# Performance work log

Hardware: AMD Instinct MI355X
Metric: run time of the kernel (lower is better)

The kernel has to match this reference:

```python
import jax, jax.numpy as jnp
import numpy as np

N = 50000
TOPK = 32
IN_C = 128
OUT_C = 64
NEG_SLOPE = 0.2
BN_EPS = 1e-5


def setup_inputs() -> dict:
    key = jax.random.key(0)
    ks = jax.random.split(key, 8)
    x = jax.random.normal(ks[0], (N, IN_C), dtype=jnp.float32)
    embedding = jax.random.normal(ks[1], (N, OUT_C), dtype=jnp.float32)
    # edges: each node has TOPK incoming edges, no self loops
    tgt = jnp.repeat(jnp.arange(N, dtype=jnp.int64), TOPK)
    off = jax.random.randint(ks[2], (N * TOPK,), 1, N, dtype=jnp.int64)
    src = (tgt + off) % N
    edge_index = jnp.stack([src, tgt], axis=0)
    lin_w = jax.random.normal(ks[3], (OUT_C, IN_C), dtype=jnp.float32) * (1.0 / np.sqrt(IN_C))
    att_i = jax.random.normal(ks[4], (1, 1, OUT_C), dtype=jnp.float32) * 0.1
    att_j = jax.random.normal(ks[5], (1, 1, OUT_C), dtype=jnp.float32) * 0.1
    att_em_i = jax.random.normal(ks[6], (1, 1, OUT_C), dtype=jnp.float32) * 0.1
    att_em_j = jax.random.normal(ks[7], (1, 1, OUT_C), dtype=jnp.float32) * 0.1
    bias = jnp.zeros((OUT_C,), dtype=jnp.float32)
    bn_gamma = jnp.ones((OUT_C,), dtype=jnp.float32)
    bn_beta = jnp.zeros((OUT_C,), dtype=jnp.float32)
    return {"x": x, "embedding": embedding, "edge_index": edge_index,
            "lin_w": lin_w, "att_i": att_i, "att_j": att_j,
            "att_em_i": att_em_i, "att_em_j": att_em_j, "bias": bias,
            "bn_gamma": bn_gamma, "bn_beta": bn_beta}


def _gnn_forward(x, embedding, lin_w, att_i, att_j, att_em_i, att_em_j,
                 bias, bn_gamma, bn_beta, src, tgt):
    n = x.shape[0]
    # linear transform: [N, heads=1, OUT_C]
    x_lin = (x @ lin_w.T).reshape(n, 1, OUT_C)
    # gather per edge (self loops already appended to src/tgt)
    x_i = x_lin[tgt]                      # [Etot, 1, C]
    x_j = x_lin[src]                      # [Etot, 1, C]
    emb_i = embedding[tgt][:, None, :]    # [Etot, 1, C]
    emb_j = embedding[src][:, None, :]
    # attention logits, eq (6)-(8)
    alpha = ((x_i * att_i).sum(-1) + (emb_i * att_em_i).sum(-1)
             + (x_j * att_j).sum(-1) + (emb_j * att_em_j).sum(-1))  # [Etot, 1]
    alpha = jnp.where(alpha >= 0, alpha, NEG_SLOPE * alpha)
    # segment softmax over incoming edges of each target node
    m = jax.ops.segment_max(alpha, tgt, num_segments=n)
    m = jnp.where(jnp.isfinite(m), m, 0.0)
    e = jnp.exp(alpha - m[tgt])
    denom = jax.ops.segment_sum(e, tgt, num_segments=n)
    alpha = e / (denom[tgt] + 1e-16)      # [Etot, 1]
    # weighted scatter-add aggregation
    msg = x_j * alpha[:, :, None]         # [Etot, 1, C]
    out = jax.ops.segment_sum(msg, tgt, num_segments=n).reshape(n, OUT_C)
    out = out + bias
    # BatchNorm1d (training-mode batch stats, biased var) + ReLU
    mu = out.mean(axis=0)
    var = ((out - mu) ** 2).mean(axis=0)
    out = (out - mu) / jnp.sqrt(var + BN_EPS) * bn_gamma + bn_beta
    return jax.nn.relu(out)


def reference(x, embedding, edge_index, lin_w, att_i, att_j, att_em_i,
              att_em_j, bias, bn_gamma, bn_beta):
    n = x.shape[0]
    loops = jnp.arange(n, dtype=edge_index.dtype)
    src = jnp.concatenate([edge_index[0], loops])
    tgt = jnp.concatenate([edge_index[1], loops])
    return _gnn_forward(x, embedding, lin_w, att_i, att_j, att_em_i,
                        att_em_j, bias, bn_gamma, bn_beta, src, tgt)
```

## Files before the change

kernel.cpp:

```cpp
#include <hip/hip_runtime.h>

#define NN 50000
#define TOPK 32
#define IN_C 128
#define OUT_C 64
#define NEG_SLOPE 0.2f
#define BN_EPS 1e-5f

#define K1_BLOCKS (NN / 16)

#define NTASK (NN / 4)
#define K2_WAVES (NTASK / 2)
#define K2_BLOCKS ((K2_WAVES + 3) / 4)

#define WS_XBF   0
#define WS_AI    (NN * 32)
#define WS_AJ    (WS_AI + NN)
#define WS_SUMS  (WS_AJ + NN)

typedef __bf16 bf16x8 __attribute__((ext_vector_type(8)));
typedef float f32x4 __attribute__((ext_vector_type(4)));
union BF8 { unsigned short u[8]; bf16x8 v; };

__device__ inline float leaky(float a) { return a >= 0.f ? a : NEG_SLOPE * a; }
__device__ inline float bl(unsigned u) { return __uint_as_float(u << 16); }
__device__ inline float bh(unsigned u) { return __uint_as_float(u & 0xffff0000u); }

__device__ inline unsigned short f2bf(float f) {
    unsigned u = __float_as_uint(f);
    unsigned r = (u + 0x7fffu + ((u >> 16) & 1u)) >> 16;
    return (unsigned short)r;
}

__global__ __launch_bounds__(256) void k1_mfma(
    const float* __restrict__ x, const float* __restrict__ emb,
    const float* __restrict__ lin_w,
    const float* __restrict__ att_i, const float* __restrict__ att_j,
    const float* __restrict__ att_em_i, const float* __restrict__ att_em_j,
    unsigned short* __restrict__ x_bf, float* __restrict__ a_i,
    float* __restrict__ a_j, float* __restrict__ sums)
{
    __shared__ float redi[16][5], redj[16][5];
    __shared__ float eredi[16][17], eredj[16][17];
    const int tid = threadIdx.x;
    if (blockIdx.x == 0 && tid < 128) sums[tid] = 0.f;

    const int lane = tid & 63;
    const int wv = tid >> 6;
    const int quad = lane >> 4;
    const int nn = lane & 15;
    const int base = blockIdx.x * 16;
    const int c = wv * 16 + nn;

    BF8 bfr[4], afr[4];
    {
        const float* wr = lin_w + (size_t)c * IN_C + quad * 8;
        const float* xr = x + (size_t)(base + nn) * IN_C + quad * 8;
#pragma unroll
        for (int s = 0; s < 4; ++s) {
            const float4 wa = *(const float4*)(wr + s * 32);
            const float4 wb = *(const float4*)(wr + s * 32 + 4);
            const float4 xa = *(const float4*)(xr + s * 32);
            const float4 xb = *(const float4*)(xr + s * 32 + 4);
            bfr[s].u[0] = f2bf(wa.x); bfr[s].u[1] = f2bf(wa.y);
            bfr[s].u[2] = f2bf(wa.z); bfr[s].u[3] = f2bf(wa.w);
            bfr[s].u[4] = f2bf(wb.x); bfr[s].u[5] = f2bf(wb.y);
            bfr[s].u[6] = f2bf(wb.z); bfr[s].u[7] = f2bf(wb.w);
            afr[s].u[0] = f2bf(xa.x); afr[s].u[1] = f2bf(xa.y);
            afr[s].u[2] = f2bf(xa.z); afr[s].u[3] = f2bf(xa.w);
            afr[s].u[4] = f2bf(xb.x); afr[s].u[5] = f2bf(xb.y);
            afr[s].u[6] = f2bf(xb.z); afr[s].u[7] = f2bf(xb.w);
        }
    }

    f32x4 acc = {0.f, 0.f, 0.f, 0.f};
#pragma unroll
    for (int s = 0; s < 4; ++s)
        acc = __builtin_amdgcn_mfma_f32_16x16x32_bf16(afr[s].v, bfr[s].v, acc,
                                                      0, 0, 0);

    const float aic = att_i[c], ajc = att_j[c];
    float pi[4], pj[4];
#pragma unroll
    for (int r = 0; r < 4; ++r) {
        const int node = base + quad * 4 + r;
        x_bf[(size_t)node * OUT_C + c] = f2bf(acc[r]);
        pi[r] = acc[r] * aic;
        pj[r] = acc[r] * ajc;
    }
#pragma unroll
    for (int d = 1; d < 16; d <<= 1) {
#pragma unroll
        for (int r = 0; r < 4; ++r) {
            pi[r] += __shfl_xor(pi[r], d, 64);
            pj[r] += __shfl_xor(pj[r], d, 64);
        }
    }
    if (nn == 0) {
#pragma unroll
        for (int r = 0; r < 4; ++r) {
            redi[quad * 4 + r][wv] = pi[r];
            redj[quad * 4 + r][wv] = pj[r];
        }
    }

    {
        const int nl = tid >> 4, c4 = tid & 15;
        const float4 e4 = ((const float4*)emb)[(size_t)(base + nl) * 16 + c4];
        const float4 i4 = ((const float4*)att_em_i)[c4];
        const float4 j4 = ((const float4*)att_em_j)[c4];
        eredi[nl][c4] = e4.x * i4.x + e4.y * i4.y + e4.z * i4.z + e4.w * i4.w;
        eredj[nl][c4] = e4.x * j4.x + e4.y * j4.y + e4.z * j4.z + e4.w * j4.w;
    }
    __syncthreads();
    if (tid < 16) {
        float si = redi[tid][0] + redi[tid][1] + redi[tid][2] + redi[tid][3];
        float sj = redj[tid][0] + redj[tid][1] + redj[tid][2] + redj[tid][3];
#pragma unroll
        for (int r = 0; r < 16; ++r) { si += eredi[tid][r]; sj += eredj[tid][r]; }
        a_i[base + tid] = si;
        a_j[base + tid] = sj;
    }
}

__global__ __launch_bounds__(256, 4) void k2_attn(
    const int* __restrict__ src,
    const uint2* __restrict__ x_bf2, const float* __restrict__ a_i,
    const float* __restrict__ a_j, const float* __restrict__ bias,
    float* __restrict__ out, float* __restrict__ sums)
{
    const int tid = threadIdx.x;
    const int lane = tid & 63;
    const int wv = tid >> 6;
    const int wavei = blockIdx.x * 4 + wv;
    const int g = lane >> 4;
    const int q = lane & 15;
    const float4 b4 = ((const float4*)bias)[q];

    float bs1[4] = {0.f, 0.f, 0.f, 0.f};
    float bs2[4] = {0.f, 0.f, 0.f, 0.f};

    if (wavei < K2_WAVES) {
#pragma unroll
        for (int r = 0; r < 2; ++r) {
            const int task = wavei + r * K2_WAVES;
            const int t = task * 4 + g;
            const float ai_t = a_i[t];
            const int4* sp4 = (const int4*)(src + (size_t)t * TOPK);

            int4 s4[8];
#pragma unroll
            for (int i = 0; i < 8; ++i) s4[i] = sp4[i];

            float alj[33];
#pragma unroll
            for (int i = 0; i < 8; ++i) {
                alj[i * 4 + 0] = a_j[s4[i].x];
                alj[i * 4 + 1] = a_j[s4[i].y];
                alj[i * 4 + 2] = a_j[s4[i].z];
                alj[i * 4 + 3] = a_j[s4[i].w];
            }
            alj[32] = a_j[t];

            float mx = -1e30f;
#pragma unroll
            for (int e = 0; e < 33; ++e) {
                alj[e] = leaky(ai_t + alj[e]);
                mx = fmaxf(mx, alj[e]);
            }
            float den = 0.f;
#pragma unroll
            for (int e = 0; e < 33; ++e) { alj[e] = __expf(alj[e] - mx); den += alj[e]; }
            const float inv = 1.f / (den + 1e-16f);

            float A0 = 0.f, A1 = 0.f, A2 = 0.f, A3 = 0.f;
#define ACC4(U, W)                                                            \
            { A0 = fmaf(W, bl(U.x), A0); A1 = fmaf(W, bh(U.x), A1);           \
              A2 = fmaf(W, bl(U.y), A2); A3 = fmaf(W, bh(U.y), A3); }
#pragma unroll
            for (int i = 0; i < 8; ++i) {
                const uint2 u0 = x_bf2[(size_t)s4[i].x * 16 + q];
                const uint2 u1 = x_bf2[(size_t)s4[i].y * 16 + q];
                const uint2 u2 = x_bf2[(size_t)s4[i].z * 16 + q];
                const uint2 u3 = x_bf2[(size_t)s4[i].w * 16 + q];
                const float w0 = alj[i * 4 + 0] * inv;
                const float w1 = alj[i * 4 + 1] * inv;
                const float w2 = alj[i * 4 + 2] * inv;
                const float w3 = alj[i * 4 + 3] * inv;
                ACC4(u0, w0); ACC4(u1, w1); ACC4(u2, w2); ACC4(u3, w3);
            }
            {
                const uint2 us = x_bf2[(size_t)t * 16 + q];
                const float wsf = alj[32] * inv;
                ACC4(us, wsf);
            }
#undef ACC4
            const float v0 = A0 + b4.x, v1 = A1 + b4.y;
            const float v2 = A2 + b4.z, v3 = A3 + b4.w;
            ((float4*)out)[t * 16 + q] = make_float4(v0, v1, v2, v3);
            bs1[0] += v0; bs1[1] += v1; bs1[2] += v2; bs1[3] += v3;
            bs2[0] = fmaf(v0, v0, bs2[0]); bs2[1] = fmaf(v1, v1, bs2[1]);
            bs2[2] = fmaf(v2, v2, bs2[2]); bs2[3] = fmaf(v3, v3, bs2[3]);
        }
    }

    __shared__ float sb1[64][17];
    __shared__ float sb2[64][17];
    const int slot = wv * 4 + g;
#pragma unroll
    for (int j = 0; j < 4; ++j) {
        sb1[q * 4 + j][slot] = bs1[j];
        sb2[q * 4 + j][slot] = bs2[j];
    }
    __syncthreads();
    if (tid < 64) {
        float t1 = 0.f, t2 = 0.f;
#pragma unroll
        for (int rr = 0; rr < 16; ++rr) { t1 += sb1[tid][rr]; t2 += sb2[tid][rr]; }
        atomicAdd(&sums[tid], t1);
        atomicAdd(&sums[64 + tid], t2);
    }
}

__global__ __launch_bounds__(256) void k4_bn(
    float* __restrict__ out, const float* __restrict__ sums,
    const float* __restrict__ gamma, const float* __restrict__ beta)
{
    __shared__ float s_sc[64], s_sh[64];
    const int tid = threadIdx.x;
    if (tid < 64) {
        const float mu = sums[tid] / (float)NN;
        const float ex2 = sums[64 + tid] / (float)NN;
        const float var = fmaxf(ex2 - mu * mu, 0.f);
        const float sc = gamma[tid] / sqrtf(var + BN_EPS);
        s_sc[tid] = sc;
        s_sh[tid] = beta[tid] - mu * sc;
    }
    __syncthreads();
    const int total = NN * OUT_C / 4;
    float4* p = (float4*)out;
    for (int idx = blockIdx.x * 256 + tid; idx < total; idx += gridDim.x * 256) {
        float4 v = p[idx];
        const int c0 = (idx & 15) * 4;
        v.x = fmaxf(fmaf(v.x, s_sc[c0 + 0], s_sh[c0 + 0]), 0.f);
        v.y = fmaxf(fmaf(v.y, s_sc[c0 + 1], s_sh[c0 + 1]), 0.f);
        v.z = fmaxf(fmaf(v.z, s_sc[c0 + 2], s_sh[c0 + 2]), 0.f);
        v.w = fmaxf(fmaf(v.w, s_sc[c0 + 3], s_sh[c0 + 3]), 0.f);
        p[idx] = v;
    }
}

extern "C" void kernel_launch(void* const* d_in, const int* in_sizes, int n_in,
                              void* d_out, int out_size, void* d_ws, size_t ws_size,
                              hipStream_t stream) {
    const float* x        = (const float*)d_in[0];
    const float* emb      = (const float*)d_in[1];
    const int*   edge     = (const int*)d_in[2];
    const float* lin_w    = (const float*)d_in[3];
    const float* att_i    = (const float*)d_in[4];
    const float* att_j    = (const float*)d_in[5];
    const float* att_em_i = (const float*)d_in[6];
    const float* att_em_j = (const float*)d_in[7];
    const float* bias     = (const float*)d_in[8];
    const float* gamma    = (const float*)d_in[9];
    const float* beta     = (const float*)d_in[10];

    float* ws    = (float*)d_ws;
    unsigned short* x_bf = (unsigned short*)(ws + WS_XBF);
    float* a_i   = ws + WS_AI;
    float* a_j   = ws + WS_AJ;
    float* sums  = ws + WS_SUMS;
    float* out   = (float*)d_out;

    k1_mfma<<<K1_BLOCKS, 256, 0, stream>>>(x, emb, lin_w, att_i, att_j,
                                           att_em_i, att_em_j, x_bf, a_i, a_j, sums);
    k2_attn<<<K2_BLOCKS, 256, 0, stream>>>(edge, (const uint2*)x_bf, a_i, a_j,
                                           bias, out, sums);
    k4_bn<<<1024, 256, 0, stream>>>(out, sums, gamma, beta);
}
```

Before: 178.1 us.

## Split attention kernel into separate softmax and aggregation kernels

Splits the fused attention kernel into two kernels. The first computes the per-node softmax weights, spread across 16 lanes with shuffle reductions, and writes them into the output buffer as scratch. The second reads those weights back and runs the bf16 gather-aggregate plus the batch-norm statistics. The aim is to cut per-thread register pressure and serial work from the 33-element softmax per lane, and to drop the two-tasks-per-wave loop. The cost is an extra kernel launch, an extra global write and read of the weights, and twice as many atomic reductions for the statistics.

Result: slower. 217.3 us (+22.1%).

```diff
diff --git a/kernel.cpp b/kernel.cpp
--- a/kernel.cpp
+++ b/kernel.cpp
@@ -9,9 +9,7 @@
 
 #define K1_BLOCKS (NN / 16)
 
-#define NTASK (NN / 4)
-#define K2_WAVES (NTASK / 2)
-#define K2_BLOCKS ((K2_WAVES + 3) / 4)
+#define K2_BLOCKS (NN / 16)
 
 #define WS_XBF   0
 #define WS_AI    (NN * 32)
@@ -103,7 +101,6 @@
             redj[quad * 4 + r][wv] = pj[r];
         }
     }
-
     {
         const int nl = tid >> 4, c4 = tid & 15;
         const float4 e4 = ((const float4*)emb)[(size_t)(base + nl) * 16 + c4];
@@ -123,100 +120,97 @@
     }
 }
 
-__global__ __launch_bounds__(256, 4) void k2_attn(
-    const int* __restrict__ src,
-    const uint2* __restrict__ x_bf2, const float* __restrict__ a_i,
-    const float* __restrict__ a_j, const float* __restrict__ bias,
-    float* __restrict__ out, float* __restrict__ sums)
+__global__ __launch_bounds__(256) void k2a_softmax(
+    const int* __restrict__ src, const float* __restrict__ a_i,
+    const float* __restrict__ a_j, float* __restrict__ out)
 {
     const int tid = threadIdx.x;
     const int lane = tid & 63;
     const int wv = tid >> 6;
-    const int wavei = blockIdx.x * 4 + wv;
     const int g = lane >> 4;
     const int q = lane & 15;
+    const int t = (blockIdx.x * 4 + wv) * 4 + g;
+
+    const float ai_t = a_i[t];
+    const int s0 = src[(size_t)t * TOPK + q];
+    const int s1 = src[(size_t)t * TOPK + 16 + q];
+    const float l0 = leaky(ai_t + a_j[s0]);
+    const float l1 = leaky(ai_t + a_j[s1]);
+    const float ls = leaky(ai_t + a_j[t]);
+
+    float m = fmaxf(l0, l1);
+#pragma unroll
+    for (int d = 1; d < 16; d <<= 1) m = fmaxf(m, __shfl_xor(m, d, 64));
+    m = fmaxf(m, ls);
+    const float e0 = __expf(l0 - m);
+    const float e1 = __expf(l1 - m);
+    const float es = __expf(ls - m);
+    float den = e0 + e1;
+#pragma unroll
+    for (int d = 1; d < 16; d <<= 1) den += __shfl_xor(den, d, 64);
+    den += es + 1e-16f;
+    const float inv = 1.f / den;
+
+    float* wrow = out + (size_t)t * OUT_C;
+    wrow[q] = e0 * inv;
+    wrow[16 + q] = e1 * inv;
+    if (q == 0) wrow[32] = es * inv;
+}
+
+__global__ __launch_bounds__(256, 2) void k2b_agg(
+    const int* __restrict__ src, const uint2* __restrict__ x_bf2,
+    const float* __restrict__ bias, float* out, float* __restrict__ sums)
+{
+    const int tid = threadIdx.x;
+    const int lane = tid & 63;
+    const int wv = tid >> 6;
+    const int g = lane >> 4;
+    const int q = lane & 15;
+    const int t = (blockIdx.x * 4 + wv) * 4 + g;
     const float4 b4 = ((const float4*)bias)[q];
 
-    float bs1[4] = {0.f, 0.f, 0.f, 0.f};
-    float bs2[4] = {0.f, 0.f, 0.f, 0.f};
-
-    if (wavei < K2_WAVES) {
-#pragma unroll
-        for (int r = 0; r < 2; ++r) {
-            const int task = wavei + r * K2_WAVES;
-            const int t = task * 4 + g;
-            const float ai_t = a_i[t];
-            const int4* sp4 = (const int4*)(src + (size_t)t * TOPK);
-
-            int4 s4[8];
-#pragma unroll
-            for (int i = 0; i < 8; ++i) s4[i] = sp4[i];
-
-            float alj[33];
-#pragma unroll
-            for (int i = 0; i < 8; ++i) {
-                alj[i * 4 + 0] = a_j[s4[i].x];
-                alj[i * 4 + 1] = a_j[s4[i].y];
-                alj[i * 4 + 2] = a_j[s4[i].z];
-                alj[i * 4 + 3] = a_j[s4[i].w];
-            }
-            alj[32] = a_j[t];
-
-            float mx = -1e30f;
-#pragma unroll
-            for (int e = 0; e < 33; ++e) {
-                alj[e] = leaky(ai_t + alj[e]);
-                mx = fmaxf(mx, alj[e]);
-            }
-            float den = 0.f;
-#pragma unroll
-            for (int e = 0; e < 33; ++e) { alj[e] = __expf(alj[e] - mx); den += alj[e]; }
-            const float inv = 1.f / (den + 1e-16f);
-
-            float A0 = 0.f, A1 = 0.f, A2 = 0.f, A3 = 0.f;
+    const float* wrow = out + (size_t)t * OUT_C;
+    float4 w4[8];
+#pragma unroll
+    for (int i = 0; i < 8; ++i) w4[i] = ((const float4*)wrow)[i];
+    const float wself = wrow[32];
+
+    const int4* sp4 = (const int4*)(src + (size_t)t * TOPK);
+    float A0 = 0.f, A1 = 0.f, A2 = 0.f, A3 = 0.f;
 #define ACC4(U, W)                                                            \
-            { A0 = fmaf(W, bl(U.x), A0); A1 = fmaf(W, bh(U.x), A1);           \
-              A2 = fmaf(W, bl(U.y), A2); A3 = fmaf(W, bh(U.y), A3); }
-#pragma unroll
-            for (int i = 0; i < 8; ++i) {
-                const uint2 u0 = x_bf2[(size_t)s4[i].x * 16 + q];
-                const uint2 u1 = x_bf2[(size_t)s4[i].y * 16 + q];
-                const uint2 u2 = x_bf2[(size_t)s4[i].z * 16 + q];
-                const uint2 u3 = x_bf2[(size_t)s4[i].w * 16 + q];
-                const float w0 = alj[i * 4 + 0] * inv;
-                const float w1 = alj[i * 4 + 1] * inv;
-                const float w2 = alj[i * 4 + 2] * inv;
-                const float w3 = alj[i * 4 + 3] * inv;
-                ACC4(u0, w0); ACC4(u1, w1); ACC4(u2, w2); ACC4(u3, w3);
-            }
-            {
-                const uint2 us = x_bf2[(size_t)t * 16 + q];
-                const float wsf = alj[32] * inv;
-                ACC4(us, wsf);
-            }
+    { A0 = fmaf(W, bl(U.x), A0); A1 = fmaf(W, bh(U.x), A1);                   \
+      A2 = fmaf(W, bl(U.y), A2); A3 = fmaf(W, bh(U.y), A3); }
+#pragma unroll
+    for (int i = 0; i < 8; ++i) {
+        const int4 s4 = sp4[i];
+        const uint2 u0 = x_bf2[(size_t)s4.x * 16 + q];
+        const uint2 u1 = x_bf2[(size_t)s4.y * 16 + q];
+        const uint2 u2 = x_bf2[(size_t)s4.z * 16 + q];
+        const uint2 u3 = x_bf2[(size_t)s4.w * 16 + q];
+        ACC4(u0, w4[i].x); ACC4(u1, w4[i].y);
+        ACC4(u2, w4[i].z); ACC4(u3, w4[i].w);
+    }
+    {
+        const uint2 us = x_bf2[(size_t)t * 16 + q];
+        ACC4(us, wself);
+    }
 #undef ACC4
-            const float v0 = A0 + b4.x, v1 = A1 + b4.y;
-            const float v2 = A2 + b4.z, v3 = A3 + b4.w;
-            ((float4*)out)[t * 16 + q] = make_float4(v0, v1, v2, v3);
-            bs1[0] += v0; bs1[1] += v1; bs1[2] += v2; bs1[3] += v3;
-            bs2[0] = fmaf(v0, v0, bs2[0]); bs2[1] = fmaf(v1, v1, bs2[1]);
-            bs2[2] = fmaf(v2, v2, bs2[2]); bs2[3] = fmaf(v3, v3, bs2[3]);
-        }
-    }
+    const float v0 = A0 + b4.x, v1 = A1 + b4.y;
+    const float v2 = A2 + b4.z, v3 = A3 + b4.w;
+    ((float4*)out)[(size_t)t * 16 + q] = make_float4(v0, v1, v2, v3);
 
     __shared__ float sb1[64][17];
     __shared__ float sb2[64][17];
     const int slot = wv * 4 + g;
-#pragma unroll
-    for (int j = 0; j < 4; ++j) {
-        sb1[q * 4 + j][slot] = bs1[j];
-        sb2[q * 4 + j][slot] = bs2[j];
-    }
+    sb1[q * 4 + 0][slot] = v0; sb1[q * 4 + 1][slot] = v1;
+    sb1[q * 4 + 2][slot] = v2; sb1[q * 4 + 3][slot] = v3;
+    sb2[q * 4 + 0][slot] = v0 * v0; sb2[q * 4 + 1][slot] = v1 * v1;
+    sb2[q * 4 + 2][slot] = v2 * v2; sb2[q * 4 + 3][slot] = v3 * v3;
     __syncthreads();
     if (tid < 64) {
         float t1 = 0.f, t2 = 0.f;
 #pragma unroll
-        for (int rr = 0; rr < 16; ++rr) { t1 += sb1[tid][rr]; t2 += sb2[tid][rr]; }
+        for (int r = 0; r < 16; ++r) { t1 += sb1[tid][r]; t2 += sb2[tid][r]; }
         atomicAdd(&sums[tid], t1);
         atomicAdd(&sums[64 + tid], t2);
     }
@@ -274,7 +268,7 @@
 
     k1_mfma<<<K1_BLOCKS, 256, 0, stream>>>(x, emb, lin_w, att_i, att_j,
                                            att_em_i, att_em_j, x_bf, a_i, a_j, sums);
-    k2_attn<<<K2_BLOCKS, 256, 0, stream>>>(edge, (const uint2*)x_bf, a_i, a_j,
-                                           bias, out, sums);
+    k2a_softmax<<<K2_BLOCKS, 256, 0, stream>>>(edge, a_i, a_j, out);
+    k2b_agg<<<K2_BLOCKS, 256, 0, stream>>>(edge, (const uint2*)x_bf, bias, out, sums);
     k4_bn<<<1024, 256, 0, stream>>>(out, sums, gamma, beta);
 }
```

## Issue all neighbor feature gathers upfront, one node group per wave

Applied to the files above, without the earlier changes.

The attention kernel now gives each 16-lane group exactly one target node instead of two per wave. All 33 bf16 neighbor-feature gathers are issued into registers before the softmax is computed, so their memory latency overlaps the a_j gathers and the exp work. The occupancy hint is removed from launch bounds. The cost is twice as many blocks, doubling the atomicAdds for the BN statistics, plus higher register pressure from holding 33 uint2 values, which may reduce occupancy.

Result: slower. 209.3 us (+17.5%).

```diff
diff --git a/kernel.cpp b/kernel.cpp
--- a/kernel.cpp
+++ b/kernel.cpp
@@ -9,9 +9,7 @@
 
 #define K1_BLOCKS (NN / 16)
 
-#define NTASK (NN / 4)
-#define K2_WAVES (NTASK / 2)
-#define K2_BLOCKS ((K2_WAVES + 3) / 4)
+#define K2_BLOCKS (NN / 16)
 
 #define WS_XBF   0
 #define WS_AI    (NN * 32)
@@ -103,7 +101,6 @@
             redj[quad * 4 + r][wv] = pj[r];
         }
     }
-
     {
         const int nl = tid >> 4, c4 = tid & 15;
         const float4 e4 = ((const float4*)emb)[(size_t)(base + nl) * 16 + c4];
@@ -123,7 +120,7 @@
     }
 }
 
-__global__ __launch_bounds__(256, 4) void k2_attn(
+__global__ __launch_bounds__(256) void k2_attn(
     const int* __restrict__ src,
     const uint2* __restrict__ x_bf2, const float* __restrict__ a_i,
     const float* __restrict__ a_j, const float* __restrict__ bias,
@@ -132,91 +129,73 @@
     const int tid = threadIdx.x;
     const int lane = tid & 63;
     const int wv = tid >> 6;
-    const int wavei = blockIdx.x * 4 + wv;
     const int g = lane >> 4;
     const int q = lane & 15;
+    const int t = (blockIdx.x * 4 + wv) * 4 + g;
     const float4 b4 = ((const float4*)bias)[q];
 
-    float bs1[4] = {0.f, 0.f, 0.f, 0.f};
-    float bs2[4] = {0.f, 0.f, 0.f, 0.f};
-
-    if (wavei < K2_WAVES) {
-#pragma unroll
-        for (int r = 0; r < 2; ++r) {
-            const int task = wavei + r * K2_WAVES;
-            const int t = task * 4 + g;
-            const float ai_t = a_i[t];
-            const int4* sp4 = (const int4*)(src + (size_t)t * TOPK);
-
-            int4 s4[8];
-#pragma unroll
-            for (int i = 0; i < 8; ++i) s4[i] = sp4[i];
-
-            float alj[33];
-#pragma unroll
-            for (int i = 0; i < 8; ++i) {
-                alj[i * 4 + 0] = a_j[s4[i].x];
-                alj[i * 4 + 1] = a_j[s4[i].y];
-                alj[i * 4 + 2] = a_j[s4[i].z];
-                alj[i * 4 + 3] = a_j[s4[i].w];
-            }
-            alj[32] = a_j[t];
-
-            float mx = -1e30f;
-#pragma unroll
-            for (int e = 0; e < 33; ++e) {
-                alj[e] = leaky(ai_t + alj[e]);
-                mx = fmaxf(mx, alj[e]);
-            }
-            float den = 0.f;
-#pragma unroll
-            for (int e = 0; e < 33; ++e) { alj[e] = __expf(alj[e] - mx); den += alj[e]; }
-            const float inv = 1.f / (den + 1e-16f);
-
-            float A0 = 0.f, A1 = 0.f, A2 = 0.f, A3 = 0.f;
-#define ACC4(U, W)                                                            \
-            { A0 = fmaf(W, bl(U.x), A0); A1 = fmaf(W, bh(U.x), A1);           \
-              A2 = fmaf(W, bl(U.y), A2); A3 = fmaf(W, bh(U.y), A3); }
-#pragma unroll
-            for (int i = 0; i < 8; ++i) {
-                const uint2 u0 = x_bf2[(size_t)s4[i].x * 16 + q];
-                const uint2 u1 = x_bf2[(size_t)s4[i].y * 16 + q];
-                const uint2 u2 = x_bf2[(size_t)s4[i].z * 16 + q];
-                const uint2 u3 = x_bf2[(size_t)s4[i].w * 16 + q];
-                const float w0 = alj[i * 4 + 0] * inv;
-                const float w1 = alj[i * 4 + 1] * inv;
-                const float w2 = alj[i * 4 + 2] * inv;
-                const float w3 = alj[i * 4 + 3] * inv;
-                ACC4(u0, w0); ACC4(u1, w1); ACC4(u2, w2); ACC4(u3, w3);
-            }
-            {
-                const uint2 us = x_bf2[(size_t)t * 16 + q];
-                const float wsf = alj[32] * inv;
-                ACC4(us, wsf);
-            }
-#undef ACC4
-            const float v0 = A0 + b4.x, v1 = A1 + b4.y;
-            const float v2 = A2 + b4.z, v3 = A3 + b4.w;
-            ((float4*)out)[t * 16 + q] = make_float4(v0, v1, v2, v3);
-            bs1[0] += v0; bs1[1] += v1; bs1[2] += v2; bs1[3] += v3;
-            bs2[0] = fmaf(v0, v0, bs2[0]); bs2[1] = fmaf(v1, v1, bs2[1]);
-            bs2[2] = fmaf(v2, v2, bs2[2]); bs2[3] = fmaf(v3, v3, bs2[3]);
-        }
-    }
+    const int4* sp4 = (const int4*)(src + (size_t)t * TOPK);
+    int4 s4[8];
+#pragma unroll
+    for (int i = 0; i < 8; ++i) s4[i] = sp4[i];
+
+    uint2 u[33];
+#pragma unroll
+    for (int i = 0; i < 8; ++i) {
+        u[i * 4 + 0] = x_bf2[(size_t)s4[i].x * 16 + q];
+        u[i * 4 + 1] = x_bf2[(size_t)s4[i].y * 16 + q];
+        u[i * 4 + 2] = x_bf2[(size_t)s4[i].z * 16 + q];
+        u[i * 4 + 3] = x_bf2[(size_t)s4[i].w * 16 + q];
+    }
+    u[32] = x_bf2[(size_t)t * 16 + q];
+
+    const float ai_t = a_i[t];
+    float alj[33];
+#pragma unroll
+    for (int i = 0; i < 8; ++i) {
+        alj[i * 4 + 0] = a_j[s4[i].x];
+        alj[i * 4 + 1] = a_j[s4[i].y];
+        alj[i * 4 + 2] = a_j[s4[i].z];
+        alj[i * 4 + 3] = a_j[s4[i].w];
+    }
+    alj[32] = a_j[t];
+
+    float mx = -1e30f;
+#pragma unroll
+    for (int e = 0; e < 33; ++e) {
+        alj[e] = leaky(ai_t + alj[e]);
+        mx = fmaxf(mx, alj[e]);
+    }
+    float den = 0.f;
+#pragma unroll
+    for (int e = 0; e < 33; ++e) { alj[e] = __expf(alj[e] - mx); den += alj[e]; }
+    const float inv = 1.f / (den + 1e-16f);
+
+    float A0 = 0.f, A1 = 0.f, A2 = 0.f, A3 = 0.f;
+#pragma unroll
+    for (int e = 0; e < 33; ++e) {
+        const float w = alj[e] * inv;
+        A0 = fmaf(w, bl(u[e].x), A0);
+        A1 = fmaf(w, bh(u[e].x), A1);
+        A2 = fmaf(w, bl(u[e].y), A2);
+        A3 = fmaf(w, bh(u[e].y), A3);
+    }
+    const float v0 = A0 + b4.x, v1 = A1 + b4.y;
+    const float v2 = A2 + b4.z, v3 = A3 + b4.w;
+    ((float4*)out)[(size_t)t * 16 + q] = make_float4(v0, v1, v2, v3);
 
     __shared__ float sb1[64][17];
     __shared__ float sb2[64][17];
     const int slot = wv * 4 + g;
-#pragma unroll
-    for (int j = 0; j < 4; ++j) {
-        sb1[q * 4 + j][slot] = bs1[j];
-        sb2[q * 4 + j][slot] = bs2[j];
-    }
+    sb1[q * 4 + 0][slot] = v0; sb1[q * 4 + 1][slot] = v1;
+    sb1[q * 4 + 2][slot] = v2; sb1[q * 4 + 3][slot] = v3;
+    sb2[q * 4 + 0][slot] = v0 * v0; sb2[q * 4 + 1][slot] = v1 * v1;
+    sb2[q * 4 + 2][slot] = v2 * v2; sb2[q * 4 + 3][slot] = v3 * v3;
     __syncthreads();
     if (tid < 64) {
         float t1 = 0.f, t2 = 0.f;
 #pragma unroll
-        for (int rr = 0; rr < 16; ++rr) { t1 += sb1[tid][rr]; t2 += sb2[tid][rr]; }
+        for (int r = 0; r < 16; ++r) { t1 += sb1[tid][r]; t2 += sb2[tid][r]; }
         atomicAdd(&sums[tid], t1);
         atomicAdd(&sums[64 + tid], t2);
     }
```
